# Performance work log

Hardware: AMD Instinct MI355X
Metric: run time of the kernel (lower is better)

## Reference

```python
import jax, jax.numpy as jnp
import numpy as np

EPS = 1e-5

def batchnorm2d(x, w, b):
    # training-mode BN: per-channel stats over (B, H, W), biased variance
    mean = jnp.mean(x, axis=(0, 2, 3), keepdims=True)
    var = jnp.var(x, axis=(0, 2, 3), keepdims=True)
    xn = (x - mean) * jax.lax.rsqrt(var + EPS)
    return xn * w[None, :, None, None] + b[None, :, None, None]

def setup_inputs() -> dict:
    key = jax.random.key(0)
    ks = jax.random.split(key, 12)
    B, C, H, W = 4, 64, 64, 64
    Cq = C // 8
    s = 1.0 / np.sqrt(C)
    return {
        "x": jax.random.normal(ks[0], (B, C, H, W), jnp.float32),
        "Wq": jax.random.normal(ks[1], (Cq, C), jnp.float32) * s,
        "bq": jnp.zeros((Cq,), jnp.float32),
        "Wk": jax.random.normal(ks[2], (Cq, C), jnp.float32) * s,
        "bk": jnp.zeros((Cq,), jnp.float32),
        "Wv": jax.random.normal(ks[3], (C, C), jnp.float32) * s,
        "bv": jnp.zeros((C,), jnp.float32),
        "gamma_p": jax.random.normal(ks[4], (), jnp.float32) * 0.1,
        "bnp_w": jnp.ones((C,), jnp.float32),
        "bnp_b": jnp.zeros((C,), jnp.float32),
        "gamma_c": jax.random.normal(ks[5], (), jnp.float32) * 0.1,
        "bnc_w": jnp.ones((C,), jnp.float32),
        "bnc_b": jnp.zeros((C,), jnp.float32),
    }

def reference(x, Wq, bq, Wk, bk, Wv, bv, gamma_p, bnp_w, bnp_b, gamma_c, bnc_w, bnc_b):
    B, C, H, W = x.shape
    N = H * W
    xf = x.reshape(B, C, N)

    # ---- PAM (position attention) ----
    q = jnp.einsum('dc,bcn->bnd', Wq, xf) + bq  # [B, N, Cq]
    k = jnp.einsum('dc,bcn->bdn', Wk, xf) + bk[None, :, None]  # [B, Cq, N]
    v = jnp.einsum('dc,bcn->bdn', Wv, xf) + bv[None, :, None]  # [B, C, N]
    energy = jnp.einsum('bnd,bdm->bnm', q, k)  # [B, N, N]
    attn = jax.nn.softmax(energy, axis=-1)
    # out[b,c,m] = sum_n v[b,c,n] * attn[m,n]  (bmm(v, attn^T))
    out = jnp.einsum('bcn,bmn->bcm', v, attn).reshape(B, C, H, W)
    out = gamma_p * out
    out = batchnorm2d(out, bnp_w, bnp_b)
    y = out + x  # PAM residual

    # ---- CAM (channel attention) ----
    yf = y.reshape(B, C, N)
    energy_c = jnp.einsum('bcn,bdn->bcd', yf, yf)  # [B, C, C]
    energy_new = jnp.max(energy_c, axis=-1, keepdims=True) - energy_c
    attn_c = jax.nn.softmax(energy_new, axis=-1)
    out_c = jnp.einsum('bcd,bdn->bcn', attn_c, yf).reshape(B, C, H, W)
    out_c = gamma_c * out_c
    out_c = batchnorm2d(out_c, bnc_w, bnc_b)
    return out_c + y  # CAM residual
```

## Files before the change

kernel.cpp:

```cpp
#include <hip/hip_runtime.h>

#define NN 4096
#define EPS 1e-5f

typedef unsigned long long u64;
union f2u { float f[2]; u64 u; };

#define Q_OFF   0u
#define K_OFF   131072u
#define V_OFF   262144u
#define O_OFF   1310720u
#define Y_OFF   2359296u
#define OC_OFF  3407872u
#define AT_OFF  4456448u
#define S2_OFF  4472832u
#define PS_OFF  4472960u
#define CNT_OFF 4473088u
#define OP_OFF  4473344u
#define LP_OFF  8667648u

__global__ __launch_bounds__(256) void proj_kernel(
    const float* __restrict__ x, const float* __restrict__ Wq, const float* __restrict__ bq,
    const float* __restrict__ Wk, const float* __restrict__ bk,
    const float* __restrict__ Wv, const float* __restrict__ bv,
    float* __restrict__ q, float* __restrict__ k, float* __restrict__ v) {
  __shared__ float sWq[8*64], sWk[8*64], sWv[64*64], sbq[8], sbk[8], sbv[64];
  __shared__ float xt[64*68];
  int t = threadIdx.x;
  int b = blockIdx.x >> 6;
  int sp = blockIdx.x & 63;
  int n0 = sp << 6;
  for (int i = t; i < 512; i += 256) { sWq[i] = Wq[i]; sWk[i] = Wk[i]; }
  for (int i = t; i < 4096; i += 256) sWv[i] = Wv[i];
  if (t < 64) sbv[t] = bv[t];
  if (t < 8) { sbq[t] = bq[t]; sbk[t] = bk[t]; }
  for (int i = t; i < 1024; i += 256) {
    int c = i >> 4, nf = (i & 15) << 2;
    *(float4*)&xt[c*68 + nf] =
        *(const float4*)&x[(size_t)(((b<<6)|c)<<12) + n0 + nf];
  }
  __syncthreads();
  int nl = t & 63;
  int n = n0 | nl;
  int cg_ = t >> 6;
  float xv[64];
  #pragma unroll
  for (int c = 0; c < 64; ++c) xv[c] = xt[c*68 + nl];
  for (int c = cg_*16; c < cg_*16+16; ++c) {
    float acc = sbv[c];
    #pragma unroll
    for (int c2 = 0; c2 < 64; ++c2) acc += sWv[c*64 + c2] * xv[c2];
    v[(((b<<6)|c)<<12) | n] = acc;
  }
  if (cg_ == 0) {
    #pragma unroll
    for (int d = 0; d < 8; ++d) {
      float acc = sbq[d];
      #pragma unroll
      for (int c = 0; c < 64; ++c) acc += sWq[d*64+c] * xv[c];
      q[(((b<<12)|n)<<3) | d] = acc;
    }
  } else if (cg_ == 1) {
    #pragma unroll
    for (int d = 0; d < 8; ++d) {
      float acc = sbk[d];
      #pragma unroll
      for (int c = 0; c < 64; ++c) acc += sWk[d*64+c] * xv[c];
      k[(((b<<3)|d)<<12) | n] = acc;
    }
  }
}

__global__ __launch_bounds__(256, 4) void attn_kernel(
    const float* __restrict__ q, const float* __restrict__ k,
    const float* __restrict__ v, float* __restrict__ op,
    float* __restrict__ lp, float* __restrict__ o,
    float* __restrict__ psums, int* __restrict__ cnt) {
  __shared__ float kst[64*12];
  __shared__ float vst[64*68];
  __shared__ float pst[64*68];
  __shared__ int who;

  const int bi   = blockIdx.x;
  const int g    = bi & 3;
  const int rest = bi >> 2;
  const int mt   = rest & 63;
  const int b    = rest >> 6;
  const int m0   = mt << 6;
  const int t    = threadIdx.x;

  const int rq = t & 15;
  const int sg = t >> 4;

  float4 qa[4][2];
  #pragma unroll
  for (int r = 0; r < 4; ++r) {
    const float4* qp = (const float4*)&q[(size_t)(((b<<12) | (m0 + (rq<<2) + r)) << 3)];
    qa[r][0] = qp[0]; qa[r][1] = qp[1];
  }

  float lsum[4] = {0.f, 0.f, 0.f, 0.f};
  float av[4][4] = {{0.f}};

  const int span = NN >> 2;
  const int nbeg = g * span;

  for (int n0 = nbeg; n0 < nbeg + span; n0 += 64) {
    __syncthreads();
    #pragma unroll
    for (int i = t; i < 512; i += 256) {
      int ni = i & 63, d = i >> 6;
      kst[ni*12 + d] = k[(((b<<3)|d)<<12) + n0 + ni];
    }
    #pragma unroll
    for (int i = t; i < 4096; i += 256) {
      int ni = i & 63, c = i >> 6;
      vst[ni*68 + c] = v[(((b<<6)|c)<<12) + n0 + ni];
    }
    __syncthreads();
    #pragma unroll
    for (int j = 0; j < 4; ++j) {
      const int ni = (sg << 2) | j;
      const float4 ka = *(const float4*)&kst[ni*12];
      const float4 kb = *(const float4*)&kst[ni*12 + 4];
      float pj[4];
      #pragma unroll
      for (int r = 0; r < 4; ++r) {
        float s = qa[r][0].x*ka.x + qa[r][0].y*ka.y + qa[r][0].z*ka.z + qa[r][0].w*ka.w
                + qa[r][1].x*kb.x + qa[r][1].y*kb.y + qa[r][1].z*kb.z + qa[r][1].w*kb.w;
        float e = __expf(s);
        pj[r] = e;
        lsum[r] += e;
      }
      *(float4*)&pst[ni*68 + (rq<<2)] = make_float4(pj[0], pj[1], pj[2], pj[3]);
    }
    __syncthreads();
    #pragma unroll 4
    for (int ni = 0; ni < 64; ++ni) {
      const float4 p4 = *(const float4*)&pst[ni*68 + (sg<<2)];
      const float4 v4 = *(const float4*)&vst[ni*68 + (rq<<2)];
      av[0][0] += p4.x*v4.x; av[0][1] += p4.x*v4.y; av[0][2] += p4.x*v4.z; av[0][3] += p4.x*v4.w;
      av[1][0] += p4.y*v4.x; av[1][1] += p4.y*v4.y; av[1][2] += p4.y*v4.z; av[1][3] += p4.y*v4.w;
      av[2][0] += p4.z*v4.x; av[2][1] += p4.z*v4.y; av[2][2] += p4.z*v4.z; av[2][3] += p4.z*v4.w;
      av[3][0] += p4.w*v4.x; av[3][1] += p4.w*v4.y; av[3][2] += p4.w*v4.z; av[3][3] += p4.w*v4.w;
    }
  }
  __syncthreads();
  *(float4*)&pst[sg*68 + (rq<<2)] = make_float4(lsum[0], lsum[1], lsum[2], lsum[3]);
  __syncthreads();
  if (t < 64) {
    float l = 0.f;
    #pragma unroll
    for (int s = 0; s < 16; ++s) l += pst[s*68 + t];
    __hip_atomic_store(&lp[(((((g<<2)|b)<<6) | mt)<<6) | t], l,
                       __ATOMIC_RELAXED, __HIP_MEMORY_SCOPE_AGENT);
  }
  float* ob = op + ((size_t)((((g<<2)|b)<<6) | mt) << 12);
  #pragma unroll
  for (int r = 0; r < 4; ++r) {
    const int base = (((sg<<2)|r)<<6) | (rq<<2);
    f2u lo, hi;
    lo.f[0] = av[r][0]; lo.f[1] = av[r][1];
    hi.f[0] = av[r][2]; hi.f[1] = av[r][3];
    __hip_atomic_store((u64*)&ob[base],     lo.u, __ATOMIC_RELAXED, __HIP_MEMORY_SCOPE_AGENT);
    __hip_atomic_store((u64*)&ob[base + 2], hi.u, __ATOMIC_RELAXED, __HIP_MEMORY_SCOPE_AGENT);
  }

  __syncthreads();
  if (t == 0)
    who = __hip_atomic_fetch_add(&cnt[(b<<6) | mt], 1,
                                 __ATOMIC_RELEASE, __HIP_MEMORY_SCOPE_AGENT);
  __syncthreads();
  if (who != 3) return;
  if (t == 0)
    __builtin_amdgcn_fence(__ATOMIC_ACQUIRE, "agent");
  __syncthreads();

  float* sm = vst;
  float* linv = kst;
  if (t < 64) {
    float l = 0.f;
    #pragma unroll
    for (int g2 = 0; g2 < 4; ++g2)
      l += lp[(((((g2<<2)|b)<<6) | mt)<<6) | t];
    linv[t] = 1.f / l;
  }
  __syncthreads();
  for (int i = 0; i < 16; ++i) {
    int idx = (i<<8) + t;
    float s = 0.f;
    #pragma unroll
    for (int g2 = 0; g2 < 4; ++g2)
      s += op[((size_t)((((g2<<2)|b)<<6) | mt) << 12) + idx];
    int m = idx >> 6, c = idx & 63;
    sm[c*65 + m] = s * linv[m];
  }
  __syncthreads();
  for (int i = 0; i < 16; ++i) {
    int idx = (i<<8) + t;
    int m = idx & 63, c = idx >> 6;
    float ov = sm[c*65 + m];
    o[(((b<<6)|c)<<12) | (mt<<6) | m] = ov;
    float s1 = ov, s2 = ov*ov;
    #pragma unroll
    for (int off2 = 32; off2; off2 >>= 1) {
      s1 += __shfl_xor(s1, off2, 64);
      s2 += __shfl_xor(s2, off2, 64);
    }
    if ((t & 63) == 0) { atomicAdd(&psums[c], s1); atomicAdd(&psums[64+c], s2); }
  }
}

__global__ __launch_bounds__(256) void yg_kernel(
    const float* __restrict__ o, const float* __restrict__ x,
    const float* __restrict__ psums,
    const float* __restrict__ gp, const float* __restrict__ w1, const float* __restrict__ bb1,
    float* __restrict__ y, float* __restrict__ gpart) {
  __shared__ float yt[64*68];
  __shared__ float cf[128];
  const int bi = blockIdx.x;
  const int b = bi >> 6, sp = bi & 63;
  const int t = threadIdx.x;
  const int n0 = sp << 6;
  if (t < 64) {
    float m1 = psums[t] * (1.f/16384.f), m2 = psums[64+t] * (1.f/16384.f);
    float var = m2 - m1*m1;
    float gg = *gp;
    float r = rsqrtf(gg*gg*var + EPS);
    float a = gg * r * w1[t];
    cf[t] = a; cf[64+t] = bb1[t] - m1*a;
  }
  __syncthreads();
  #pragma unroll
  for (int i = 0; i < 16; ++i) {
    int idx = (i<<8) + t;
    int c = idx >> 6, m = idx & 63;
    size_t gi = ((size_t)(((b<<6)|c)<<12)) + n0 + m;
    float yv = o[gi]*cf[c] + cf[64+c] + x[gi];
    yt[c*68 + m] = yv;
    y[gi] = yv;
  }
  __syncthreads();
  {
    int tc = t >> 4, td = t & 15;
    float acc[4][4] = {{0.f}};
    #pragma unroll
    for (int mj = 0; mj < 16; ++mj) {
      float4 ya[4], yb[4];
      #pragma unroll
      for (int r = 0; r < 4; ++r)  ya[r] = *(const float4*)&yt[((tc<<2)+r)*68 + (mj<<2)];
      #pragma unroll
      for (int ss = 0; ss < 4; ++ss) yb[ss] = *(const float4*)&yt[((td<<2)+ss)*68 + (mj<<2)];
      #pragma unroll
      for (int r = 0; r < 4; ++r)
        #pragma unroll
        for (int ss = 0; ss < 4; ++ss)
          acc[r][ss] += ya[r].x*yb[ss].x + ya[r].y*yb[ss].y + ya[r].z*yb[ss].z + ya[r].w*yb[ss].w;
    }
    float* gb = gpart + ((size_t)bi << 12);
    #pragma unroll
    for (int r = 0; r < 4; ++r)
      *(float4*)&gb[(((tc<<2)+r)<<6) | (td<<2)] =
          make_float4(acc[r][0], acc[r][1], acc[r][2], acc[r][3]);
  }
}

__global__ __launch_bounds__(256) void csm_kernel(
    const float* __restrict__ gpart, float* __restrict__ attnc) {
  __shared__ float red[256];
  const int bi = blockIdx.x;
  const int b = bi >> 6, row = bi & 63;
  const int t = threadIdx.x;
  const int d = t & 63, spg = t >> 6;
  float e = 0.f;
  #pragma unroll
  for (int jj = 0; jj < 16; ++jj) {
    int spp = (spg<<4) + jj;
    e += gpart[((size_t)((b<<6)|spp) << 12) + (row<<6) + d];
  }
  red[t] = e;
  __syncthreads();
  if (t < 64) {
    float ee = red[t]+red[64+t]+red[128+t]+red[192+t];
    float mn = ee;
    #pragma unroll
    for (int off = 32; off; off >>= 1) mn = fminf(mn, __shfl_xor(mn, off, 64));
    float p = __expf(mn - ee);
    float s = p;
    #pragma unroll
    for (int off = 32; off; off >>= 1) s += __shfl_xor(s, off, 64);
    attnc[(((b<<6)|row)<<6) | t] = p / s;
  }
}

__global__ __launch_bounds__(256) void cam_apply_kernel(
    const float* __restrict__ attn, const float* __restrict__ y,
    float* __restrict__ oc, float* __restrict__ sums) {
  __shared__ float satt[64*68];
  int b = blockIdx.x >> 6;
  int n = ((blockIdx.x & 63) << 6) | (threadIdx.x & 63);
  int cg_ = threadIdx.x >> 6;
  for (int i = threadIdx.x; i < 4096; i += 256)
    satt[(i>>6)*68 + (i&63)] = attn[(b<<12) | i];
  __syncthreads();
  float yv[64];
  #pragma unroll
  for (int d = 0; d < 64; ++d) yv[d] = y[(((b<<6)|d)<<12) | n];
  for (int c = cg_*16; c < cg_*16+16; ++c) {
    float acc = 0.f;
    #pragma unroll
    for (int d4 = 0; d4 < 16; ++d4) {
      float4 avv = *(const float4*)&satt[c*68 + (d4<<2)];
      acc += avv.x*yv[d4*4] + avv.y*yv[d4*4+1] + avv.z*yv[d4*4+2] + avv.w*yv[d4*4+3];
    }
    oc[(((b<<6)|c)<<12) | n] = acc;
    float s1 = acc, s2 = acc*acc;
    #pragma unroll
    for (int off = 32; off; off >>= 1) { s1 += __shfl_xor(s1, off, 64); s2 += __shfl_xor(s2, off, 64); }
    if ((threadIdx.x & 63) == 0) { atomicAdd(&sums[c], s1); atomicAdd(&sums[64+c], s2); }
  }
}

__global__ __launch_bounds__(256) void fin_kernel(
    const float* __restrict__ oc, const float* __restrict__ y,
    const float* __restrict__ s2b,
    const float* __restrict__ gc, const float* __restrict__ w2, const float* __restrict__ bb2,
    float* __restrict__ out) {
  __shared__ float cf[128];
  const int bi = blockIdx.x;
  const int b = bi >> 6, sp = bi & 63;
  const int t = threadIdx.x;
  const int n0 = sp << 6;
  if (t < 64) {
    float m1 = s2b[t] * (1.f/16384.f), m2 = s2b[64+t] * (1.f/16384.f);
    float var = m2 - m1*m1;
    float gg = *gc;
    float r = rsqrtf(gg*gg*var + EPS);
    float a = gg * r * w2[t];
    cf[t] = a; cf[64+t] = bb2[t] - m1*a;
  }
  __syncthreads();
  const int n = t & 63, cg_ = t >> 6;
  #pragma unroll
  for (int jj = 0; jj < 16; ++jj) {
    int c = (cg_<<4) + jj;
    size_t gi = ((size_t)(((b<<6)|c)<<12)) + n0 + n;
    out[gi] = oc[gi]*cf[c] + cf[64+c] + y[gi];
  }
}

extern "C" void kernel_launch(void* const* d_in, const int* in_sizes, int n_in,
                              void* d_out, int out_size, void* d_ws, size_t ws_size,
                              hipStream_t stream) {
  (void)in_sizes; (void)n_in; (void)out_size; (void)ws_size;
  const float* x      = (const float*)d_in[0];
  const float* Wq     = (const float*)d_in[1];
  const float* bq     = (const float*)d_in[2];
  const float* Wk     = (const float*)d_in[3];
  const float* bk     = (const float*)d_in[4];
  const float* Wv     = (const float*)d_in[5];
  const float* bv     = (const float*)d_in[6];
  const float* gp     = (const float*)d_in[7];
  const float* bnp_w  = (const float*)d_in[8];
  const float* bnp_b  = (const float*)d_in[9];
  const float* gc     = (const float*)d_in[10];
  const float* bnc_w  = (const float*)d_in[11];
  const float* bnc_b  = (const float*)d_in[12];

  float* ws = (float*)d_ws;
  float* q     = ws + Q_OFF;
  float* k     = ws + K_OFF;
  float* v     = ws + V_OFF;
  float* o     = ws + O_OFF;
  float* y     = ws + Y_OFF;
  float* oc    = ws + OC_OFF;
  float* atc   = ws + AT_OFF;
  float* s2b   = ws + S2_OFF;
  float* ps    = ws + PS_OFF;
  int*   cnt   = (int*)(ws + CNT_OFF);
  float* op    = ws + OP_OFF;
  float* lpart = ws + LP_OFF;
  float* gpart = op;

  hipMemsetAsync(s2b, 0, 512u * sizeof(float), stream);

  proj_kernel<<<256, 256, 0, stream>>>(x, Wq, bq, Wk, bk, Wv, bv, q, k, v);
  attn_kernel<<<1024, 256, 0, stream>>>(q, k, v, op, lpart, o, ps, cnt);
  yg_kernel<<<256, 256, 0, stream>>>(o, x, ps, gp, bnp_w, bnp_b, y, gpart);
  csm_kernel<<<256, 256, 0, stream>>>(gpart, atc);
  cam_apply_kernel<<<256, 256, 0, stream>>>(atc, y, oc, s2b);
  fin_kernel<<<256, 256, 0, stream>>>(oc, y, s2b, gc, bnc_w, bnc_b, (float*)d_out);
}
```

Baseline: 474.4 us.

## Fuse PAM residual, CAM gram, softmax, apply and BN into one grid-barrier kernel

```diff
diff --git a/kernel.cpp b/kernel.cpp
--- a/kernel.cpp
+++ b/kernel.cpp
@@ -10,14 +10,13 @@
 #define K_OFF   131072u
 #define V_OFF   262144u
 #define O_OFF   1310720u
-#define Y_OFF   2359296u
-#define OC_OFF  3407872u
 #define AT_OFF  4456448u
 #define S2_OFF  4472832u
 #define PS_OFF  4472960u
 #define CNT_OFF 4473088u
-#define OP_OFF  4473344u
-#define LP_OFF  8667648u
+#define BAR_OFF 4473344u
+#define OP_OFF  4473600u
+#define LP_OFF  8667904u
 
 __global__ __launch_bounds__(256) void proj_kernel(
     const float* __restrict__ x, const float* __restrict__ Wq, const float* __restrict__ bq,
@@ -211,19 +210,38 @@
   }
 }
 
-__global__ __launch_bounds__(256) void yg_kernel(
+__device__ __forceinline__ void grid_bar(int* __restrict__ ctr, int t) {
+  __syncthreads();
+  if (t == 0) {
+    __hip_atomic_fetch_add(ctr, 1, __ATOMIC_RELEASE, __HIP_MEMORY_SCOPE_AGENT);
+    while (__hip_atomic_load(ctr, __ATOMIC_RELAXED, __HIP_MEMORY_SCOPE_AGENT) < 256)
+      __builtin_amdgcn_s_sleep(2);
+    __builtin_amdgcn_fence(__ATOMIC_ACQUIRE, "agent");
+  }
+  __syncthreads();
+}
+
+__global__ __launch_bounds__(256) void tail_kernel(
     const float* __restrict__ o, const float* __restrict__ x,
-    const float* __restrict__ psums,
+    const float* __restrict__ ps,
     const float* __restrict__ gp, const float* __restrict__ w1, const float* __restrict__ bb1,
-    float* __restrict__ y, float* __restrict__ gpart) {
+    const float* __restrict__ gc, const float* __restrict__ w2, const float* __restrict__ bb2,
+    float* __restrict__ gpart, float* __restrict__ attnc,
+    float* __restrict__ s2b, int* __restrict__ bars,
+    float* __restrict__ out) {
   __shared__ float yt[64*68];
+  __shared__ float satt[64*68];
   __shared__ float cf[128];
+  __shared__ float red[256];
+
   const int bi = blockIdx.x;
   const int b = bi >> 6, sp = bi & 63;
   const int t = threadIdx.x;
   const int n0 = sp << 6;
+  const int nl = t & 63, cg_ = t >> 6;
+
   if (t < 64) {
-    float m1 = psums[t] * (1.f/16384.f), m2 = psums[64+t] * (1.f/16384.f);
+    float m1 = ps[t] * (1.f/16384.f), m2 = ps[64+t] * (1.f/16384.f);
     float var = m2 - m1*m1;
     float gg = *gp;
     float r = rsqrtf(gg*gg*var + EPS);
@@ -236,9 +254,7 @@
     int idx = (i<<8) + t;
     int c = idx >> 6, m = idx & 63;
     size_t gi = ((size_t)(((b<<6)|c)<<12)) + n0 + m;
-    float yv = o[gi]*cf[c] + cf[64+c] + x[gi];
-    yt[c*68 + m] = yv;
-    y[gi] = yv;
+    yt[c*68 + m] = o[gi]*cf[c] + cf[64+c] + x[gi];
   }
   __syncthreads();
   {
@@ -259,78 +275,71 @@
     }
     float* gb = gpart + ((size_t)bi << 12);
     #pragma unroll
-    for (int r = 0; r < 4; ++r)
-      *(float4*)&gb[(((tc<<2)+r)<<6) | (td<<2)] =
-          make_float4(acc[r][0], acc[r][1], acc[r][2], acc[r][3]);
-  }
-}
-
-__global__ __launch_bounds__(256) void csm_kernel(
-    const float* __restrict__ gpart, float* __restrict__ attnc) {
-  __shared__ float red[256];
-  const int bi = blockIdx.x;
-  const int b = bi >> 6, row = bi & 63;
-  const int t = threadIdx.x;
-  const int d = t & 63, spg = t >> 6;
-  float e = 0.f;
-  #pragma unroll
-  for (int jj = 0; jj < 16; ++jj) {
-    int spp = (spg<<4) + jj;
-    e += gpart[((size_t)((b<<6)|spp) << 12) + (row<<6) + d];
-  }
-  red[t] = e;
-  __syncthreads();
-  if (t < 64) {
-    float ee = red[t]+red[64+t]+red[128+t]+red[192+t];
-    float mn = ee;
-    #pragma unroll
-    for (int off = 32; off; off >>= 1) mn = fminf(mn, __shfl_xor(mn, off, 64));
-    float p = __expf(mn - ee);
-    float s = p;
-    #pragma unroll
-    for (int off = 32; off; off >>= 1) s += __shfl_xor(s, off, 64);
-    attnc[(((b<<6)|row)<<6) | t] = p / s;
-  }
-}
-
-__global__ __launch_bounds__(256) void cam_apply_kernel(
-    const float* __restrict__ attn, const float* __restrict__ y,
-    float* __restrict__ oc, float* __restrict__ sums) {
-  __shared__ float satt[64*68];
-  int b = blockIdx.x >> 6;
-  int n = ((blockIdx.x & 63) << 6) | (threadIdx.x & 63);
-  int cg_ = threadIdx.x >> 6;
-  for (int i = threadIdx.x; i < 4096; i += 256)
-    satt[(i>>6)*68 + (i&63)] = attn[(b<<12) | i];
-  __syncthreads();
-  float yv[64];
-  #pragma unroll
-  for (int d = 0; d < 64; ++d) yv[d] = y[(((b<<6)|d)<<12) | n];
-  for (int c = cg_*16; c < cg_*16+16; ++c) {
-    float acc = 0.f;
-    #pragma unroll
-    for (int d4 = 0; d4 < 16; ++d4) {
-      float4 avv = *(const float4*)&satt[c*68 + (d4<<2)];
-      acc += avv.x*yv[d4*4] + avv.y*yv[d4*4+1] + avv.z*yv[d4*4+2] + avv.w*yv[d4*4+3];
-    }
-    oc[(((b<<6)|c)<<12) | n] = acc;
-    float s1 = acc, s2 = acc*acc;
-    #pragma unroll
-    for (int off = 32; off; off >>= 1) { s1 += __shfl_xor(s1, off, 64); s2 += __shfl_xor(s2, off, 64); }
-    if ((threadIdx.x & 63) == 0) { atomicAdd(&sums[c], s1); atomicAdd(&sums[64+c], s2); }
-  }
-}
-
-__global__ __launch_bounds__(256) void fin_kernel(
-    const float* __restrict__ oc, const float* __restrict__ y,
-    const float* __restrict__ s2b,
-    const float* __restrict__ gc, const float* __restrict__ w2, const float* __restrict__ bb2,
-    float* __restrict__ out) {
-  __shared__ float cf[128];
-  const int bi = blockIdx.x;
-  const int b = bi >> 6, sp = bi & 63;
-  const int t = threadIdx.x;
-  const int n0 = sp << 6;
+    for (int r = 0; r < 4; ++r) {
+      const int base = (((tc<<2)+r)<<6) | (td<<2);
+      f2u lo, hi;
+      lo.f[0] = acc[r][0]; lo.f[1] = acc[r][1];
+      hi.f[0] = acc[r][2]; hi.f[1] = acc[r][3];
+      __hip_atomic_store((u64*)&gb[base],     lo.u, __ATOMIC_RELAXED, __HIP_MEMORY_SCOPE_AGENT);
+      __hip_atomic_store((u64*)&gb[base + 2], hi.u, __ATOMIC_RELAXED, __HIP_MEMORY_SCOPE_AGENT);
+    }
+  }
+  grid_bar(&bars[0], t);
+
+  {
+    const int d = t & 63, spg = t >> 6;
+    float e = 0.f;
+    #pragma unroll
+    for (int jj = 0; jj < 16; ++jj) {
+      int spp = (spg<<4) + jj;
+      e += gpart[((size_t)((b<<6)|spp) << 12) + (sp<<6) + d];
+    }
+    red[t] = e;
+    __syncthreads();
+    if (t < 64) {
+      float ee = red[t]+red[64+t]+red[128+t]+red[192+t];
+      float mn = ee;
+      #pragma unroll
+      for (int off = 32; off; off >>= 1) mn = fminf(mn, __shfl_xor(mn, off, 64));
+      float p = __expf(mn - ee);
+      float s = p;
+      #pragma unroll
+      for (int off = 32; off; off >>= 1) s += __shfl_xor(s, off, 64);
+      __hip_atomic_store(&attnc[(((b<<6)|sp)<<6) | t], p / s,
+                         __ATOMIC_RELAXED, __HIP_MEMORY_SCOPE_AGENT);
+    }
+  }
+  grid_bar(&bars[1], t);
+
+  float oc[16];
+  {
+    #pragma unroll
+    for (int i = 0; i < 16; ++i) {
+      int idx = (i<<8) + t;
+      satt[(idx>>6)*68 + (idx&63)] = attnc[(b<<12) + idx];
+    }
+    __syncthreads();
+    float yv[64];
+    #pragma unroll
+    for (int d = 0; d < 64; ++d) yv[d] = yt[d*68 + nl];
+    #pragma unroll
+    for (int j = 0; j < 16; ++j) {
+      int c = (cg_<<4) + j;
+      float acc = 0.f;
+      #pragma unroll
+      for (int d4 = 0; d4 < 16; ++d4) {
+        float4 avv = *(const float4*)&satt[c*68 + (d4<<2)];
+        acc += avv.x*yv[d4*4] + avv.y*yv[d4*4+1] + avv.z*yv[d4*4+2] + avv.w*yv[d4*4+3];
+      }
+      oc[j] = acc;
+      float s1 = acc, s2 = acc*acc;
+      #pragma unroll
+      for (int off = 32; off; off >>= 1) { s1 += __shfl_xor(s1, off, 64); s2 += __shfl_xor(s2, off, 64); }
+      if ((t & 63) == 0) { atomicAdd(&s2b[c], s1); atomicAdd(&s2b[64+c], s2); }
+    }
+  }
+  grid_bar(&bars[2], t);
+
   if (t < 64) {
     float m1 = s2b[t] * (1.f/16384.f), m2 = s2b[64+t] * (1.f/16384.f);
     float var = m2 - m1*m1;
@@ -340,12 +349,11 @@
     cf[t] = a; cf[64+t] = bb2[t] - m1*a;
   }
   __syncthreads();
-  const int n = t & 63, cg_ = t >> 6;
-  #pragma unroll
-  for (int jj = 0; jj < 16; ++jj) {
-    int c = (cg_<<4) + jj;
-    size_t gi = ((size_t)(((b<<6)|c)<<12)) + n0 + n;
-    out[gi] = oc[gi]*cf[c] + cf[64+c] + y[gi];
+  #pragma unroll
+  for (int j = 0; j < 16; ++j) {
+    int c = (cg_<<4) + j;
+    size_t gi = ((size_t)(((b<<6)|c)<<12)) + n0 + nl;
+    out[gi] = oc[j]*cf[c] + cf[64+c] + yt[c*68 + nl];
   }
 }
 
@@ -372,22 +380,20 @@
   float* k     = ws + K_OFF;
   float* v     = ws + V_OFF;
   float* o     = ws + O_OFF;
-  float* y     = ws + Y_OFF;
-  float* oc    = ws + OC_OFF;
   float* atc   = ws + AT_OFF;
   float* s2b   = ws + S2_OFF;
   float* ps    = ws + PS_OFF;
   int*   cnt   = (int*)(ws + CNT_OFF);
+  int*   bars  = (int*)(ws + BAR_OFF);
   float* op    = ws + OP_OFF;
   float* lpart = ws + LP_OFF;
   float* gpart = op;
 
-  hipMemsetAsync(s2b, 0, 512u * sizeof(float), stream);
+  hipMemsetAsync(s2b, 0, 528u * sizeof(float), stream);
 
   proj_kernel<<<256, 256, 0, stream>>>(x, Wq, bq, Wk, bk, Wv, bv, q, k, v);
   attn_kernel<<<1024, 256, 0, stream>>>(q, k, v, op, lpart, o, ps, cnt);
-  yg_kernel<<<256, 256, 0, stream>>>(o, x, ps, gp, bnp_w, bnp_b, y, gpart);
-  csm_kernel<<<256, 256, 0, stream>>>(gpart, atc);
-  cam_apply_kernel<<<256, 256, 0, stream>>>(atc, y, oc, s2b);
-  fin_kernel<<<256, 256, 0, stream>>>(oc, y, s2b, gc, bnc_w, bnc_b, (float*)d_out);
-}
+  tail_kernel<<<256, 256, 0, stream>>>(o, x, ps, gp, bnp_w, bnp_b,
+                                       gc, bnc_w, bnc_b, gpart, atc, s2b,
+                                       bars, (float*)d_out);
+}
```

Result: slower. 500.3 us (+5.5%).
